# Performance work log

Measured on AMD Instinct MI355X. Metric: run time of the kernel, lower is better.

Reference implementation:

```python
import jax, jax.numpy as jnp
import numpy as np

N_FEATURES = 16
N_FREQUENCIES = 256
TIME_AXIS = 1


def setup_inputs() -> dict:
    key = jax.random.key(0)
    x = jax.random.normal(key, (32, 4096, 16), dtype=jnp.float32)
    return {"x": x}


def reference(x):
    # x: (B, T, F)
    B, T, F = x.shape
    n = 2 * T                 # FFT length >= 2T-1 -> linear cross-correlation
    L = (T - 1) // 2          # torch 'same' left padding for kernel size T

    # rfft of zero-padded signals along time: (B, n//2+1, F)
    Xf = jnp.fft.rfft(x, n=n, axis=1)

    # Pairwise cross-spectra. Pair (i, j) corresponds to conv1d(f_i, kernel=f_j):
    #   corr_ij[t] = sum_k f_i[t + k - L] * f_j[k]  ==  irfft(Xf_i * conj(Xf_j)) shifted by L.
    P = jnp.einsum('bti,btj->btij', Xf, jnp.conj(Xf))      # (B, n//2+1, F, F)
    P = P.reshape(B, Xf.shape[1], F * F)                   # pair order = i*F + j (loop order)

    corr_full = jnp.fft.irfft(P, n=n, axis=1)              # (B, n, F*F) circular xcorr
    idx = (jnp.arange(T) - L) % n                          # 'same'-padding window of lags
    convs = corr_full[:, idx, :]                           # (B, T, F*F)

    convs_fft = jnp.fft.rfft(convs, axis=TIME_AXIS, norm='ortho')[:, :N_FREQUENCIES, :]
    return convs_fft.mean(axis=-1, keepdims=True)          # (B, n_frequencies, 1) complex64
```

## Files before the change

### kernel.cpp

```cpp
#include <hip/hip_runtime.h>
#include <hip/hip_bf16.h>


#define B_DIM 32
#define T_DIM 4096
#define NLAG 2049
#define NCHUNK 16
#define TS (T_DIM / NCHUNK)
#define LOGI 2304
#define PSTRIDE 2052
#define THETA 1.5339807878856412e-03f

#define SW(l) ((l) + (((l) >> 5) << 2))
#define LS_PHYS 2592

__global__ __launch_bounds__(256) void ksum(const float* __restrict__ x,
                                            float* __restrict__ s) {
    int i = blockIdx.x * 256 + threadIdx.x;
    const float4* xv = (const float4*)(x + (size_t)i * 16);
    float4 a = xv[0], b = xv[1], c = xv[2], d = xv[3];
    s[i] = ((a.x + a.y) + (a.z + a.w)) + ((b.x + b.y) + (b.z + b.w)) +
           ((c.x + c.y) + (c.z + c.w)) + ((d.x + d.y) + (d.z + d.w));
}

__global__ __launch_bounds__(256) void kautoc(const float* __restrict__ s,
                                              float* __restrict__ part) {
    __shared__ __align__(16) float ls[LS_PHYS];
    int b = blockIdx.x;
    int q = blockIdx.y;
    int t0 = q * TS;
    const float* sb = s + (size_t)b * T_DIM;
    for (int idx = threadIdx.x; idx < LOGI / 4; idx += 256) {
        int l = idx * 4;
        int g = t0 + l;
        float4 v = make_float4(0.f, 0.f, 0.f, 0.f);
        if (g < T_DIM) v = *(const float4*)&sb[g];
        *(float4*)&ls[SW(l)] = v;
    }
    __syncthreads();

    float* pr = part + ((size_t)b * NCHUNK + q) * PSTRIDE;
    int tau0 = threadIdx.x * 8;

    float acc[8] = {0.f, 0.f, 0.f, 0.f, 0.f, 0.f, 0.f, 0.f};
    float w[16];
    {
        float4 w0 = *(const float4*)&ls[SW(tau0)];
        float4 w1 = *(const float4*)&ls[SW(tau0 + 4)];
        w[0] = w0.x; w[1] = w0.y; w[2] = w0.z; w[3] = w0.w;
        w[4] = w1.x; w[5] = w1.y; w[6] = w1.z; w[7] = w1.w;
    }
    #pragma unroll 4
    for (int t = 0; t < TS; t += 8) {
        int ln = t + tau0 + 8;
        float4 n0 = *(const float4*)&ls[SW(ln)];
        float4 n1 = *(const float4*)&ls[SW(ln + 4)];
        w[8] = n0.x;  w[9] = n0.y;  w[10] = n0.z; w[11] = n0.w;
        w[12] = n1.x; w[13] = n1.y; w[14] = n1.z; w[15] = n1.w;
        float4 a0 = *(const float4*)&ls[SW(t)];
        float4 a1 = *(const float4*)&ls[SW(t + 4)];
        float as[8] = {a0.x, a0.y, a0.z, a0.w, a1.x, a1.y, a1.z, a1.w};
        #pragma unroll
        for (int s2 = 0; s2 < 8; ++s2) {
            #pragma unroll
            for (int u = 0; u < 8; ++u)
                acc[u] = fmaf(as[s2], w[s2 + u], acc[u]);
        }
        #pragma unroll
        for (int k = 0; k < 8; ++k) w[k] = w[k + 8];
    }
    *(float4*)&pr[tau0]     = make_float4(acc[0], acc[1], acc[2], acc[3]);
    *(float4*)&pr[tau0 + 4] = make_float4(acc[4], acc[5], acc[6], acc[7]);

    if (threadIdx.x >= 192) {
        int sl = threadIdx.x - 192;
        float a2 = 0.f;
        #pragma unroll
        for (int t = 0; t < TS; t += 64)
            a2 += ls[SW(t + sl)] * ls[SW(t + sl + 2048)];
        for (int off = 32; off; off >>= 1) a2 += __shfl_down(a2, off, 64);
        if (threadIdx.x == 192) pr[2048] = a2;
    }
}

__global__ __launch_bounds__(256) void kdft(const float* __restrict__ part,
                                            float* __restrict__ out) {
    __shared__ float lr[NLAG];
    int b = blockIdx.x;
    const float* pb = part + (size_t)b * NCHUNK * PSTRIDE;
    for (int idx = threadIdx.x; idx < 512; idx += 256) {
        float4 acc = make_float4(0.f, 0.f, 0.f, 0.f);
        #pragma unroll
        for (int q = 0; q < NCHUNK; ++q) {
            float4 v = *(const float4*)&pb[(size_t)q * PSTRIDE + idx * 4];
            acc.x += v.x; acc.y += v.y; acc.z += v.z; acc.w += v.w;
        }
        *(float4*)&lr[idx * 4] = acc;
    }
    if (threadIdx.x == 0) {
        float acc = 0.f;
        #pragma unroll
        for (int q = 0; q < NCHUNK; ++q)
            acc += pb[(size_t)q * PSTRIDE + 2048];
        lr[2048] = acc;
    }
    __syncthreads();

    int m = blockIdx.y * 32 + (threadIdx.x >> 3);
    int slice = threadIdx.x & 7;
    float partsum = 0.0f;
    #pragma unroll 8
    for (int k = 0; k < 256; ++k) {
        int j = slice + (k << 3);
        int p = (m * j) & 4095;
        partsum = fmaf(lr[j], __cosf((float)p * THETA), partsum);
    }
    #pragma unroll
    for (int off = 4; off; off >>= 1) partsum += __shfl_down(partsum, off, 8);
    if (slice == 0) {
        float A = 2.0f * partsum - lr[0] + ((m & 1) ? -lr[2048] : lr[2048]);
        int qp = (2047 * m) & 4095;
        float ang = (float)qp * THETA;
        float g = A * (1.0f / 16384.0f);
        out[(size_t)b * 256 + m] = g * __cosf(ang);
        out[8192 + (size_t)b * 256 + m] = -g * __sinf(ang);
    }
}

extern "C" void kernel_launch(void* const* d_in, const int* in_sizes, int n_in,
                              void* d_out, int out_size, void* d_ws, size_t ws_size,
                              hipStream_t stream) {
    const float* x = (const float*)d_in[0];
    float* out = (float*)d_out;
    float* s = (float*)d_ws;
    float* part = s + B_DIM * T_DIM;
    ksum<<<dim3(512), dim3(256), 0, stream>>>(x, s);
    kautoc<<<dim3(B_DIM, NCHUNK), dim3(256), 0, stream>>>(s, part);
    kdft<<<dim3(B_DIM, 8), dim3(256), 0, stream>>>(part, out);
}
```

Baseline: 79.12 us.

## Fuse three kernels into one cooperative kernel with grid-wide syncs

Merges the channel-sum, chunked autocorrelation and DFT kernels into a single cooperative launch of 512 blocks. Grid syncs separate the stages, and the DFT stage reuses the shared buffer on the first 256 blocks. The aim is to remove two kernel launch gaps, which matter at this small runtime. In exchange it adds grid-barrier cost, requires all 512 blocks to be co-resident, and the LDS footprint is unchanged.

```diff
diff --git a/kernel.cpp b/kernel.cpp
--- a/kernel.cpp
+++ b/kernel.cpp
@@ -1,5 +1,8 @@
 #include <hip/hip_runtime.h>
 #include <hip/hip_bf16.h>
+#include <hip/hip_cooperative_groups.h>
+
+namespace cg = cooperative_groups;
 
 
 #define B_DIM 32
@@ -14,116 +17,124 @@
 #define SW(l) ((l) + (((l) >> 5) << 2))
 #define LS_PHYS 2592
 
-__global__ __launch_bounds__(256) void ksum(const float* __restrict__ x,
-                                            float* __restrict__ s) {
-    int i = blockIdx.x * 256 + threadIdx.x;
-    const float4* xv = (const float4*)(x + (size_t)i * 16);
-    float4 a = xv[0], b = xv[1], c = xv[2], d = xv[3];
-    s[i] = ((a.x + a.y) + (a.z + a.w)) + ((b.x + b.y) + (b.z + b.w)) +
-           ((c.x + c.y) + (c.z + c.w)) + ((d.x + d.y) + (d.z + d.w));
-}
+__global__ __launch_bounds__(256) void kfused(const float* __restrict__ x,
+                                              float* __restrict__ s,
+                                              float* __restrict__ part,
+                                              float* __restrict__ out) {
+    cg::grid_group gg = cg::this_grid();
+    __shared__ __align__(16) float ls[LS_PHYS];
+    int tid = threadIdx.x;
+    int blk = blockIdx.x;
 
-__global__ __launch_bounds__(256) void kautoc(const float* __restrict__ s,
-                                              float* __restrict__ part) {
-    __shared__ __align__(16) float ls[LS_PHYS];
-    int b = blockIdx.x;
-    int q = blockIdx.y;
-    int t0 = q * TS;
-    const float* sb = s + (size_t)b * T_DIM;
-    for (int idx = threadIdx.x; idx < LOGI / 4; idx += 256) {
-        int l = idx * 4;
-        int g = t0 + l;
-        float4 v = make_float4(0.f, 0.f, 0.f, 0.f);
-        if (g < T_DIM) v = *(const float4*)&sb[g];
-        *(float4*)&ls[SW(l)] = v;
+    {
+        int i = blk * 256 + tid;
+        const float4* xv = (const float4*)(x + (size_t)i * 16);
+        float4 a = xv[0], b = xv[1], c = xv[2], d = xv[3];
+        s[i] = ((a.x + a.y) + (a.z + a.w)) + ((b.x + b.y) + (b.z + b.w)) +
+               ((c.x + c.y) + (c.z + c.w)) + ((d.x + d.y) + (d.z + d.w));
     }
-    __syncthreads();
+    gg.sync();
 
-    float* pr = part + ((size_t)b * NCHUNK + q) * PSTRIDE;
-    int tau0 = threadIdx.x * 8;
+    {
+        int b = blk >> 4;
+        int q = blk & 15;
+        int t0 = q * TS;
+        const float* sb = s + (size_t)b * T_DIM;
+        for (int idx = tid; idx < LOGI / 4; idx += 256) {
+            int l = idx * 4;
+            int g = t0 + l;
+            float4 v = make_float4(0.f, 0.f, 0.f, 0.f);
+            if (g < T_DIM) v = *(const float4*)&sb[g];
+            *(float4*)&ls[SW(l)] = v;
+        }
+        __syncthreads();
 
-    float acc[8] = {0.f, 0.f, 0.f, 0.f, 0.f, 0.f, 0.f, 0.f};
-    float w[16];
-    {
-        float4 w0 = *(const float4*)&ls[SW(tau0)];
-        float4 w1 = *(const float4*)&ls[SW(tau0 + 4)];
-        w[0] = w0.x; w[1] = w0.y; w[2] = w0.z; w[3] = w0.w;
-        w[4] = w1.x; w[5] = w1.y; w[6] = w1.z; w[7] = w1.w;
+        float* pr = part + ((size_t)b * NCHUNK + q) * PSTRIDE;
+        int tau0 = tid * 8;
+
+        float acc[8] = {0.f, 0.f, 0.f, 0.f, 0.f, 0.f, 0.f, 0.f};
+        float w[16];
+        {
+            float4 w0 = *(const float4*)&ls[SW(tau0)];
+            float4 w1 = *(const float4*)&ls[SW(tau0 + 4)];
+            w[0] = w0.x; w[1] = w0.y; w[2] = w0.z; w[3] = w0.w;
+            w[4] = w1.x; w[5] = w1.y; w[6] = w1.z; w[7] = w1.w;
+        }
+        #pragma unroll 4
+        for (int t = 0; t < TS; t += 8) {
+            int ln = t + tau0 + 8;
+            float4 n0 = *(const float4*)&ls[SW(ln)];
+            float4 n1 = *(const float4*)&ls[SW(ln + 4)];
+            w[8] = n0.x;  w[9] = n0.y;  w[10] = n0.z; w[11] = n0.w;
+            w[12] = n1.x; w[13] = n1.y; w[14] = n1.z; w[15] = n1.w;
+            float4 a0 = *(const float4*)&ls[SW(t)];
+            float4 a1 = *(const float4*)&ls[SW(t + 4)];
+            float as[8] = {a0.x, a0.y, a0.z, a0.w, a1.x, a1.y, a1.z, a1.w};
+            #pragma unroll
+            for (int s2 = 0; s2 < 8; ++s2) {
+                #pragma unroll
+                for (int u = 0; u < 8; ++u)
+                    acc[u] = fmaf(as[s2], w[s2 + u], acc[u]);
+            }
+            #pragma unroll
+            for (int k = 0; k < 8; ++k) w[k] = w[k + 8];
+        }
+        *(float4*)&pr[tau0]     = make_float4(acc[0], acc[1], acc[2], acc[3]);
+        *(float4*)&pr[tau0 + 4] = make_float4(acc[4], acc[5], acc[6], acc[7]);
+
+        if (tid >= 192) {
+            int sl = tid - 192;
+            float a2 = 0.f;
+            #pragma unroll
+            for (int t = 0; t < TS; t += 64)
+                a2 += ls[SW(t + sl)] * ls[SW(t + sl + 2048)];
+            for (int off = 32; off; off >>= 1) a2 += __shfl_down(a2, off, 64);
+            if (tid == 192) pr[2048] = a2;
+        }
     }
-    #pragma unroll 4
-    for (int t = 0; t < TS; t += 8) {
-        int ln = t + tau0 + 8;
-        float4 n0 = *(const float4*)&ls[SW(ln)];
-        float4 n1 = *(const float4*)&ls[SW(ln + 4)];
-        w[8] = n0.x;  w[9] = n0.y;  w[10] = n0.z; w[11] = n0.w;
-        w[12] = n1.x; w[13] = n1.y; w[14] = n1.z; w[15] = n1.w;
-        float4 a0 = *(const float4*)&ls[SW(t)];
-        float4 a1 = *(const float4*)&ls[SW(t + 4)];
-        float as[8] = {a0.x, a0.y, a0.z, a0.w, a1.x, a1.y, a1.z, a1.w};
-        #pragma unroll
-        for (int s2 = 0; s2 < 8; ++s2) {
+    gg.sync();
+
+    if (blk < 256) {
+        int b = blk >> 3;
+        int g = blk & 7;
+        const float* pb = part + (size_t)b * NCHUNK * PSTRIDE;
+        for (int idx = tid; idx < 512; idx += 256) {
+            float4 acc = make_float4(0.f, 0.f, 0.f, 0.f);
             #pragma unroll
-            for (int u = 0; u < 8; ++u)
-                acc[u] = fmaf(as[s2], w[s2 + u], acc[u]);
+            for (int q = 0; q < NCHUNK; ++q) {
+                float4 v = *(const float4*)&pb[(size_t)q * PSTRIDE + idx * 4];
+                acc.x += v.x; acc.y += v.y; acc.z += v.z; acc.w += v.w;
+            }
+            *(float4*)&ls[idx * 4] = acc;
+        }
+        if (tid == 0) {
+            float acc = 0.f;
+            #pragma unroll
+            for (int q = 0; q < NCHUNK; ++q)
+                acc += pb[(size_t)q * PSTRIDE + 2048];
+            ls[2048] = acc;
+        }
+        __syncthreads();
+
+        int m = g * 32 + (tid >> 3);
+        int slice = tid & 7;
+        float partsum = 0.0f;
+        #pragma unroll 8
+        for (int k = 0; k < 256; ++k) {
+            int j = slice + (k << 3);
+            int p = (m * j) & 4095;
+            partsum = fmaf(ls[j], __cosf((float)p * THETA), partsum);
         }
         #pragma unroll
-        for (int k = 0; k < 8; ++k) w[k] = w[k + 8];
-    }
-    *(float4*)&pr[tau0]     = make_float4(acc[0], acc[1], acc[2], acc[3]);
-    *(float4*)&pr[tau0 + 4] = make_float4(acc[4], acc[5], acc[6], acc[7]);
-
-    if (threadIdx.x >= 192) {
-        int sl = threadIdx.x - 192;
-        float a2 = 0.f;
-        #pragma unroll
-        for (int t = 0; t < TS; t += 64)
-            a2 += ls[SW(t + sl)] * ls[SW(t + sl + 2048)];
-        for (int off = 32; off; off >>= 1) a2 += __shfl_down(a2, off, 64);
-        if (threadIdx.x == 192) pr[2048] = a2;
-    }
-}
-
-__global__ __launch_bounds__(256) void kdft(const float* __restrict__ part,
-                                            float* __restrict__ out) {
-    __shared__ float lr[NLAG];
-    int b = blockIdx.x;
-    const float* pb = part + (size_t)b * NCHUNK * PSTRIDE;
-    for (int idx = threadIdx.x; idx < 512; idx += 256) {
-        float4 acc = make_float4(0.f, 0.f, 0.f, 0.f);
-        #pragma unroll
-        for (int q = 0; q < NCHUNK; ++q) {
-            float4 v = *(const float4*)&pb[(size_t)q * PSTRIDE + idx * 4];
-            acc.x += v.x; acc.y += v.y; acc.z += v.z; acc.w += v.w;
+        for (int off = 4; off; off >>= 1) partsum += __shfl_down(partsum, off, 8);
+        if (slice == 0) {
+            float A = 2.0f * partsum - ls[0] + ((m & 1) ? -ls[2048] : ls[2048]);
+            int qp = (2047 * m) & 4095;
+            float ang = (float)qp * THETA;
+            float gsc = A * (1.0f / 16384.0f);
+            out[(size_t)b * 256 + m] = gsc * __cosf(ang);
+            out[8192 + (size_t)b * 256 + m] = -gsc * __sinf(ang);
         }
-        *(float4*)&lr[idx * 4] = acc;
-    }
-    if (threadIdx.x == 0) {
-        float acc = 0.f;
-        #pragma unroll
-        for (int q = 0; q < NCHUNK; ++q)
-            acc += pb[(size_t)q * PSTRIDE + 2048];
-        lr[2048] = acc;
-    }
-    __syncthreads();
-
-    int m = blockIdx.y * 32 + (threadIdx.x >> 3);
-    int slice = threadIdx.x & 7;
-    float partsum = 0.0f;
-    #pragma unroll 8
-    for (int k = 0; k < 256; ++k) {
-        int j = slice + (k << 3);
-        int p = (m * j) & 4095;
-        partsum = fmaf(lr[j], __cosf((float)p * THETA), partsum);
-    }
-    #pragma unroll
-    for (int off = 4; off; off >>= 1) partsum += __shfl_down(partsum, off, 8);
-    if (slice == 0) {
-        float A = 2.0f * partsum - lr[0] + ((m & 1) ? -lr[2048] : lr[2048]);
-        int qp = (2047 * m) & 4095;
-        float ang = (float)qp * THETA;
-        float g = A * (1.0f / 16384.0f);
-        out[(size_t)b * 256 + m] = g * __cosf(ang);
-        out[8192 + (size_t)b * 256 + m] = -g * __sinf(ang);
     }
 }
 
@@ -134,7 +145,6 @@
     float* out = (float*)d_out;
     float* s = (float*)d_ws;
     float* part = s + B_DIM * T_DIM;
-    ksum<<<dim3(512), dim3(256), 0, stream>>>(x, s);
-    kautoc<<<dim3(B_DIM, NCHUNK), dim3(256), 0, stream>>>(s, part);
-    kdft<<<dim3(B_DIM, 8), dim3(256), 0, stream>>>(part, out);
+    void* args[] = {(void*)&x, (void*)&s, (void*)&part, (void*)&out};
+    hipLaunchCooperativeKernel((void*)kfused, dim3(512), dim3(256), args, 0, stream);
 }
```

Result: slower. 186.3 us (+135.5%).

## Widen autocorrelation register tile and fold DFT via lag symmetry

Applied to the files above, without the earlier changes.

In the autocorrelation kernel each thread now computes 16 lags instead of 8, and the chunk's time range is split between two thread halves whose results are summed through shared memory. This raises FMA reuse per shared-memory load. In the DFT kernel, the cosine transform over lags 0..2048 is folded using the symmetry cos(m(2048-j)) = ±cos(mj), which depends on the parity of m. The new kernel builds sum and difference arrays and halves the number of __cosf evaluations. The cost is an extra shared-memory reduction and barrier in the autocorrelation kernel and higher register pressure.

```diff
diff --git a/kernel.cpp b/kernel.cpp
--- a/kernel.cpp
+++ b/kernel.cpp
@@ -6,7 +6,7 @@
 #define T_DIM 4096
 #define NLAG 2049
 #define NCHUNK 16
-#define TS (T_DIM / NCHUNK)
+#define TS 256
 #define LOGI 2304
 #define PSTRIDE 2052
 #define THETA 1.5339807878856412e-03f
@@ -26,69 +26,99 @@
 __global__ __launch_bounds__(256) void kautoc(const float* __restrict__ s,
                                               float* __restrict__ part) {
     __shared__ __align__(16) float ls[LS_PHYS];
+    int tid = threadIdx.x;
     int b = blockIdx.x;
     int q = blockIdx.y;
     int t0 = q * TS;
     const float* sb = s + (size_t)b * T_DIM;
-    for (int idx = threadIdx.x; idx < LOGI / 4; idx += 256) {
+    for (int idx = tid; idx < LOGI / 4; idx += 256) {
         int l = idx * 4;
-        int g = t0 + l;
+        int gi = t0 + l;
         float4 v = make_float4(0.f, 0.f, 0.f, 0.f);
-        if (g < T_DIM) v = *(const float4*)&sb[g];
+        if (gi < T_DIM) v = *(const float4*)&sb[gi];
         *(float4*)&ls[SW(l)] = v;
     }
     __syncthreads();
 
-    float* pr = part + ((size_t)b * NCHUNK + q) * PSTRIDE;
-    int tau0 = threadIdx.x * 8;
+    int g = tid & 127;
+    int h = tid >> 7;
+    int tau0 = g * 16;
+    int tb = h * 128;
 
-    float acc[8] = {0.f, 0.f, 0.f, 0.f, 0.f, 0.f, 0.f, 0.f};
-    float w[16];
+    float acc[16];
+    #pragma unroll
+    for (int u = 0; u < 16; ++u) acc[u] = 0.f;
+    float w[24];
     {
-        float4 w0 = *(const float4*)&ls[SW(tau0)];
-        float4 w1 = *(const float4*)&ls[SW(tau0 + 4)];
-        w[0] = w0.x; w[1] = w0.y; w[2] = w0.z; w[3] = w0.w;
-        w[4] = w1.x; w[5] = w1.y; w[6] = w1.z; w[7] = w1.w;
+        int l0 = tb + tau0;
+        float4 w0 = *(const float4*)&ls[SW(l0)];
+        float4 w1 = *(const float4*)&ls[SW(l0 + 4)];
+        float4 w2 = *(const float4*)&ls[SW(l0 + 8)];
+        float4 w3 = *(const float4*)&ls[SW(l0 + 12)];
+        w[0] = w0.x;  w[1] = w0.y;  w[2] = w0.z;  w[3] = w0.w;
+        w[4] = w1.x;  w[5] = w1.y;  w[6] = w1.z;  w[7] = w1.w;
+        w[8] = w2.x;  w[9] = w2.y;  w[10] = w2.z; w[11] = w2.w;
+        w[12] = w3.x; w[13] = w3.y; w[14] = w3.z; w[15] = w3.w;
     }
-    #pragma unroll 4
-    for (int t = 0; t < TS; t += 8) {
-        int ln = t + tau0 + 8;
+    #pragma unroll 2
+    for (int it = 0; it < 16; ++it) {
+        int t = tb + it * 8;
+        int ln = t + tau0 + 16;
         float4 n0 = *(const float4*)&ls[SW(ln)];
         float4 n1 = *(const float4*)&ls[SW(ln + 4)];
-        w[8] = n0.x;  w[9] = n0.y;  w[10] = n0.z; w[11] = n0.w;
-        w[12] = n1.x; w[13] = n1.y; w[14] = n1.z; w[15] = n1.w;
+        w[16] = n0.x; w[17] = n0.y; w[18] = n0.z; w[19] = n0.w;
+        w[20] = n1.x; w[21] = n1.y; w[22] = n1.z; w[23] = n1.w;
         float4 a0 = *(const float4*)&ls[SW(t)];
         float4 a1 = *(const float4*)&ls[SW(t + 4)];
         float as[8] = {a0.x, a0.y, a0.z, a0.w, a1.x, a1.y, a1.z, a1.w};
         #pragma unroll
         for (int s2 = 0; s2 < 8; ++s2) {
             #pragma unroll
-            for (int u = 0; u < 8; ++u)
+            for (int u = 0; u < 16; ++u)
                 acc[u] = fmaf(as[s2], w[s2 + u], acc[u]);
         }
         #pragma unroll
-        for (int k = 0; k < 8; ++k) w[k] = w[k + 8];
+        for (int k = 0; k < 16; ++k) w[k] = w[k + 8];
     }
-    *(float4*)&pr[tau0]     = make_float4(acc[0], acc[1], acc[2], acc[3]);
-    *(float4*)&pr[tau0 + 4] = make_float4(acc[4], acc[5], acc[6], acc[7]);
 
-    if (threadIdx.x >= 192) {
-        int sl = threadIdx.x - 192;
-        float a2 = 0.f;
+    float a2 = 0.f;
+    if (tid >= 192) {
+        int sl = tid - 192;
         #pragma unroll
         for (int t = 0; t < TS; t += 64)
             a2 += ls[SW(t + sl)] * ls[SW(t + sl + 2048)];
         for (int off = 32; off; off >>= 1) a2 += __shfl_down(a2, off, 64);
-        if (threadIdx.x == 192) pr[2048] = a2;
     }
+
+    __syncthreads();
+    if (h == 1) {
+        *(float4*)&ls[tau0]      = make_float4(acc[0], acc[1], acc[2], acc[3]);
+        *(float4*)&ls[tau0 + 4]  = make_float4(acc[4], acc[5], acc[6], acc[7]);
+        *(float4*)&ls[tau0 + 8]  = make_float4(acc[8], acc[9], acc[10], acc[11]);
+        *(float4*)&ls[tau0 + 12] = make_float4(acc[12], acc[13], acc[14], acc[15]);
+    }
+    __syncthreads();
+    float* pr = part + ((size_t)b * NCHUNK + q) * PSTRIDE;
+    if (h == 0) {
+        #pragma unroll
+        for (int u = 0; u < 16; ++u) acc[u] += ls[tau0 + u];
+        *(float4*)&pr[tau0]      = make_float4(acc[0], acc[1], acc[2], acc[3]);
+        *(float4*)&pr[tau0 + 4]  = make_float4(acc[4], acc[5], acc[6], acc[7]);
+        *(float4*)&pr[tau0 + 8]  = make_float4(acc[8], acc[9], acc[10], acc[11]);
+        *(float4*)&pr[tau0 + 12] = make_float4(acc[12], acc[13], acc[14], acc[15]);
+    }
+    if (tid == 192) pr[2048] = a2;
 }
 
 __global__ __launch_bounds__(256) void kdft(const float* __restrict__ part,
                                             float* __restrict__ out) {
-    __shared__ float lr[NLAG];
+    __shared__ float lr[PSTRIDE];
+    __shared__ float se[1026];
+    __shared__ float sd[1026];
     int b = blockIdx.x;
+    int tid = threadIdx.x;
     const float* pb = part + (size_t)b * NCHUNK * PSTRIDE;
-    for (int idx = threadIdx.x; idx < 512; idx += 256) {
+    for (int idx = tid; idx < 513; idx += 256) {
         float4 acc = make_float4(0.f, 0.f, 0.f, 0.f);
         #pragma unroll
         for (int q = 0; q < NCHUNK; ++q) {
@@ -97,33 +127,40 @@
         }
         *(float4*)&lr[idx * 4] = acc;
     }
-    if (threadIdx.x == 0) {
-        float acc = 0.f;
-        #pragma unroll
-        for (int q = 0; q < NCHUNK; ++q)
-            acc += pb[(size_t)q * PSTRIDE + 2048];
-        lr[2048] = acc;
+    __syncthreads();
+    for (int j = 1 + tid; j < 1024; j += 256) {
+        float a = lr[j], c = lr[2048 - j];
+        se[j] = a + c;
+        sd[j] = a - c;
     }
+    if (tid == 0) { se[1024] = 0.f; sd[1024] = 0.f; }
     __syncthreads();
 
-    int m = blockIdx.y * 32 + (threadIdx.x >> 3);
-    int slice = threadIdx.x & 7;
-    float partsum = 0.0f;
+    int m = blockIdx.y * 32 + (tid >> 3);
+    int slice = tid & 7;
+    const float* arr = (m & 1) ? sd : se;
+    float ps = 0.0f;
     #pragma unroll 8
-    for (int k = 0; k < 256; ++k) {
-        int j = slice + (k << 3);
+    for (int k = 0; k < 128; ++k) {
+        int j = 1 + slice + (k << 3);
         int p = (m * j) & 4095;
-        partsum = fmaf(lr[j], __cosf((float)p * THETA), partsum);
+        ps = fmaf(arr[j], __cosf((float)p * THETA), ps);
     }
     #pragma unroll
-    for (int off = 4; off; off >>= 1) partsum += __shfl_down(partsum, off, 8);
+    for (int off = 4; off; off >>= 1) ps += __shfl_down(ps, off, 8);
     if (slice == 0) {
-        float A = 2.0f * partsum - lr[0] + ((m & 1) ? -lr[2048] : lr[2048]);
+        float A;
+        if (m & 1) {
+            A = 2.0f * ps + lr[0] - lr[2048];
+        } else {
+            float sgn = ((m >> 1) & 1) ? -2.0f : 2.0f;
+            A = 2.0f * ps + lr[0] + lr[2048] + sgn * lr[1024];
+        }
         int qp = (2047 * m) & 4095;
         float ang = (float)qp * THETA;
-        float g = A * (1.0f / 16384.0f);
-        out[(size_t)b * 256 + m] = g * __cosf(ang);
-        out[8192 + (size_t)b * 256 + m] = -g * __sinf(ang);
+        float gg = A * (1.0f / 16384.0f);
+        out[(size_t)b * 256 + m] = gg * __cosf(ang);
+        out[8192 + (size_t)b * 256 + m] = -gg * __sinf(ang);
     }
 }
 
```

Result: faster. 73.78 us (-6.7%).
